# Performance work log

Measured on AMD Instinct MI355X. Metric: run time of the kernel, lower is better.

Reference implementation:

```python
import jax, jax.numpy as jnp
import numpy as np

HEAD, STACK = 8, 2
EPS = 1e-5


def _ln2d(x):
    # F.layer_norm(x, x.size()[1:]): normalize over (seq, feature) jointly, no affine
    m = jnp.mean(x, axis=(1, 2), keepdims=True)
    v = jnp.var(x, axis=(1, 2), keepdims=True)
    return (x - m) / jnp.sqrt(v + EPS)


def setup_inputs() -> dict:
    key = jax.random.key(0)
    ks = jax.random.split(key, 8)
    B, S, V, E, D, C = 64, 1024, 8000, 200, 200, 31
    g = lambda k, shape, sc: (jax.random.normal(k, shape, jnp.float32) * sc)
    return dict(
        x=jax.random.randint(ks[0], (B, S), 0, V),
        embed=g(ks[1], (V, E), 0.02),
        pos=g(ks[2], (S, E), 0.02),
        Wp=g(ks[3], (E, D), 0.05), bp=jnp.zeros((D,), jnp.float32),
        Wm=g(ks[4], (D * HEAD, D), 0.05), bm=jnp.zeros((D,), jnp.float32),
        W1=g(ks[5], (D, D), 0.05), b1=jnp.zeros((D,), jnp.float32),
        W2=g(ks[6], (D, D), 0.05), b2=jnp.zeros((D,), jnp.float32),
        Wd=g(ks[7], (D, C), 0.05), bd=jnp.zeros((C,), jnp.float32),
    )


def reference(x, embed, pos, Wp, bp, Wm, bm, W1, b1, W2, b2, Wd, bd):
    h = embed[x] + pos                       # [B,S,200]
    scale = jnp.sqrt(jnp.asarray(Wp.shape[1], jnp.float32))
    for _ in range(STACK):                   # weights shared across stacks (aliased in torch)
        r = h
        p = h @ Wp + bp                      # q = k = v (same aliased Linear in torch)
        a = jax.nn.softmax(jnp.einsum('bsd,btd->bst', p, p) / scale, axis=-1)
        c = jnp.einsum('bst,btd->bsd', a, p)  # [B,S,200]
        cat = jnp.tile(c, (1, 1, HEAD))       # all heads identical -> concat = tile
        h = _ln2d(cat @ Wm + bm + r)
        r = h
        ff = jax.nn.relu(h @ W1 + b1) @ W2 + b2
        h = _ln2d(ff + r)
    return h[:, -1, :] @ Wd + bd             # [B, class_num]; dropout = identity (eval)
```

## Files before the change

### kernel.cpp

```cpp
#include <hip/hip_runtime.h>
#include <cstddef>
#include <cstdint>
#include <cmath>

#define BDIM  64
#define SDIM  1024
#define DDIM  200
#define DPAD  224
#define PSTRIDE 232
#define CDIM  31
#define NSTACK 2
#define EPS   1e-5f
#define LN_N  204800.0f
#define PREP_BLOCKS 196

typedef __attribute__((ext_vector_type(8))) short short8;
typedef __attribute__((ext_vector_type(4))) short short4_t;
typedef __attribute__((ext_vector_type(4))) float f32x4;

__device__ __forceinline__ short f2bf(float f) {
    union { float f; unsigned u; } v; v.f = f;
    unsigned r = v.u + 0x7FFFu + ((v.u >> 16) & 1u);
    return (short)(r >> 16);
}
__device__ __forceinline__ float bf2f(short s) {
    union { unsigned u; float f; } v; v.u = ((unsigned)(unsigned short)s) << 16;
    return v.f;
}
__device__ __forceinline__ unsigned cvtpk_bf16(float a, float b) {
    unsigned r;
    asm volatile("v_cvt_pk_bf16_f32 %0, %1, %2" : "=v"(r) : "v"(a), "v"(b));
    return r;
}
__device__ __forceinline__ void gload_lds16(const short* g, short* l) {
    __builtin_amdgcn_global_load_lds(
        (const __attribute__((address_space(1))) void*)g,
        (__attribute__((address_space(3))) void*)l, 16, 0, 0);
}

__global__ void prep_embed_kernel(const int* __restrict__ x, const float* __restrict__ embed,
                                  const float* __restrict__ pos,
                                  const float* __restrict__ Wp, const float* __restrict__ bp,
                                  const float* __restrict__ Wm, const float* __restrict__ bm,
                                  const float* __restrict__ W1, const float* __restrict__ b1,
                                  const float* __restrict__ W2, const float* __restrict__ b2,
                                  short* __restrict__ WtP, short* __restrict__ WtM,
                                  short* __restrict__ Wt1, short* __restrict__ Wt2,
                                  float* __restrict__ bpP, float* __restrict__ bmP,
                                  float* __restrict__ b1P, float* __restrict__ b2P,
                                  float* __restrict__ csP, float* __restrict__ cs1,
                                  short* __restrict__ h, float* __restrict__ parts)
{
    if (blockIdx.x < PREP_BLOCKS) {
        int idx = blockIdx.x * 256 + threadIdx.x;
        if (idx >= DPAD * DPAD) return;
        int n = idx / DPAD, k = idx - n * DPAD;
        bool valid = (n < DDIM) && (k < DDIM);
        WtP[idx] = valid ? f2bf(Wp[(size_t)k * DDIM + n]) : 0;
        Wt1[idx] = valid ? f2bf(W1[(size_t)k * DDIM + n]) : 0;
        Wt2[idx] = valid ? f2bf(W2[(size_t)k * DDIM + n]) : 0;
        float s = 0.f;
        if (valid) {
            #pragma unroll
            for (int blk = 0; blk < 8; ++blk)
                s += Wm[(size_t)(blk * DDIM + k) * DDIM + n];
        }
        WtM[idx] = valid ? f2bf(s) : 0;
        if (idx < DPAD) {
            bpP[idx] = idx < DDIM ? bp[idx] : 0.f;
            bmP[idx] = idx < DDIM ? bm[idx] : 0.f;
            b1P[idx] = idx < DDIM ? b1[idx] : 0.f;
            b2P[idx] = idx < DDIM ? b2[idx] : 0.f;
            float sp = 0.f, s1 = 0.f;
            if (idx < DDIM) {
                for (int kk = 0; kk < DDIM; ++kk) {
                    sp += bf2f(f2bf(Wp[(size_t)kk * DDIM + idx]));
                    s1 += bf2f(f2bf(W1[(size_t)kk * DDIM + idx]));
                }
            }
            csP[idx] = sp;
            cs1[idx] = s1;
        }
        return;
    }

    const int eb = blockIdx.x - PREP_BLOCKS;
    if (eb == 0) {
        for (int i = threadIdx.x; i < 4 * BDIM * 2; i += 256) parts[i] = 0.f;
    }
    const int total = BDIM * SDIM * (DPAD / 4);
    for (int i = eb * 256 + threadIdx.x; i < total; i += 2048 * 256) {
        const int row = i / (DPAD / 4);
        const int n0  = (i - row * (DPAD / 4)) * 4;
        short4_t o;
        if (n0 >= DDIM) {
            o[0] = o[1] = o[2] = o[3] = 0;
        } else {
            const int s = row & (SDIM - 1);
            const int tok = x[row];
            const float4 e  = *(const float4*)(embed + (size_t)tok * DDIM + n0);
            const float4 p4 = *(const float4*)(pos + (size_t)s * DDIM + n0);
            o[0] = f2bf(e.x + p4.x); o[1] = f2bf(e.y + p4.y);
            o[2] = f2bf(e.z + p4.z); o[3] = f2bf(e.w + p4.w);
        }
        *(short4_t*)(h + (size_t)row * DPAD + n0) = o;
    }
}

#define WSLICE 7168
__global__ __launch_bounds__(256, 3)
void gemm_bf(const short* __restrict__ act, const float* __restrict__ actParts,
             const short* __restrict__ Wt, const float* __restrict__ bias,
             const float* __restrict__ csW,
             const short* __restrict__ res, const float* __restrict__ resParts,
             short* __restrict__ out, short* __restrict__ pt,
             float* __restrict__ parts, int doRelu, int outStride)
{
    __shared__ short WB[2][WSLICE];

    const int tid  = threadIdx.x;
    const int wave = tid >> 6, lane = tid & 63;
    const int lo   = lane & 15, hi = lane >> 4;
    const int mblk = blockIdx.x * 128;
    const int m0   = mblk + wave * 32;

    auto stage = [&](int ks, int buf) {
        for (int c = wave; c < 14; c += 4) {
            int row = c * 16 + (lane >> 2);
            int kc  = (lane & 3) ^ ((row >> 1) & 3);
            gload_lds16(Wt + (size_t)row * DPAD + ks * 32 + kc * 8,
                        &WB[buf][c * 512 + lane * 8]);
        }
    };

    f32x4 acc[2][14];
    #pragma unroll
    for (int mt = 0; mt < 2; ++mt)
        #pragma unroll
        for (int nt = 0; nt < 14; ++nt) acc[mt][nt] = (f32x4){0.f, 0.f, 0.f, 0.f};

    short8 af[2], afn[2];
    #pragma unroll
    for (int mt = 0; mt < 2; ++mt)
        af[mt] = *(const short8*)(act + (size_t)(m0 + mt * 16 + lo) * DPAD + hi * 8);
    stage(0, 0);
    __syncthreads();

    #pragma unroll
    for (int ks = 0; ks < 7; ++ks) {
        const int cur = ks & 1;
        if (ks < 6) {
            #pragma unroll
            for (int mt = 0; mt < 2; ++mt)
                afn[mt] = *(const short8*)(act + (size_t)(m0 + mt * 16 + lo) * DPAD
                                           + (ks + 1) * 32 + hi * 8);
            stage(ks + 1, cur ^ 1);
        }
        #pragma unroll
        for (int nt = 0; nt < 14; ++nt) {
            int brow = nt * 16 + lo;
            short8 bf_ = *(const short8*)&WB[cur][brow * 32
                                                  + ((hi * 8) ^ (((brow >> 1) & 3) << 3))];
            acc[0][nt] = __builtin_amdgcn_mfma_f32_16x16x32_bf16(af[0], bf_, acc[0][nt], 0, 0, 0);
            acc[1][nt] = __builtin_amdgcn_mfma_f32_16x16x32_bf16(af[1], bf_, acc[1][nt], 0, 0, 0);
        }
        __syncthreads();
        if (ks < 6) { af[0] = afn[0]; af[1] = afn[1]; }
    }

    const int bb = mblk >> 10;
    float inv_a = 1.f, corr = 0.f;
    if (actParts) {
        float mean = actParts[bb * 2] / LN_N;
        inv_a = rsqrtf(actParts[bb * 2 + 1] / LN_N - mean * mean + EPS);
        corr = mean * inv_a;
    }
    float mean_r = 0.f, inv_r = 1.f;
    if (resParts) {
        mean_r = resParts[bb * 2] / LN_N;
        inv_r = rsqrtf(resParts[bb * 2 + 1] / LN_N - mean_r * mean_r + EPS);
    }

    float s = 0.f, s2 = 0.f;
    #pragma unroll
    for (int mt = 0; mt < 2; ++mt) {
        #pragma unroll
        for (int nt = 0; nt < 14; ++nt) {
            const int n = nt * 16 + lo;
            const float bn = bias[n];
            const float cw = actParts ? csW[n] : 0.f;
            float v[4];
            #pragma unroll
            for (int r = 0; r < 4; ++r)
                v[r] = acc[mt][nt][r] * inv_a + bn - corr * cw;
            if (res) {
                #pragma unroll
                for (int r = 0; r < 4; ++r) {
                    int m = m0 + mt * 16 + hi * 4 + r;
                    v[r] += (bf2f(res[(size_t)m * DPAD + n]) - mean_r) * inv_r;
                }
            }
            if (doRelu)
                #pragma unroll
                for (int r = 0; r < 4; ++r) v[r] = fmaxf(v[r], 0.f);
            if (n >= DDIM)
                #pragma unroll
                for (int r = 0; r < 4; ++r) v[r] = 0.f;
            if (parts)
                #pragma unroll
                for (int r = 0; r < 4; ++r) { s += v[r]; s2 = fmaf(v[r], v[r], s2); }
            short4_t o4;
            #pragma unroll
            for (int r = 0; r < 4; ++r) o4[r] = f2bf(v[r]);
            #pragma unroll
            for (int r = 0; r < 4; ++r) {
                int m = m0 + mt * 16 + hi * 4 + r;
                out[(size_t)m * outStride + n] = o4[r];
            }
            if (pt && nt < 13) {
                const int sloc = (m0 + mt * 16 + hi * 4) & (SDIM - 1);
                *(short4_t*)(pt + ((size_t)bb * DPAD + n) * SDIM + sloc) = o4;
            }
        }
    }

    if (parts) {
        __shared__ float rs[4], rq[4];
        #pragma unroll
        for (int off = 32; off; off >>= 1) {
            s  += __shfl_down(s, off);
            s2 += __shfl_down(s2, off);
        }
        if (lane == 0) { rs[wave] = s; rq[wave] = s2; }
        __syncthreads();
        if (tid == 0) {
            atomicAdd(&parts[bb * 2],     rs[0] + rs[1] + rs[2] + rs[3]);
            atomicAdd(&parts[bb * 2 + 1], rq[0] + rq[1] + rq[2] + rq[3]);
        }
    }
}

#define Y1S 232
__global__ __launch_bounds__(256, 2)
void ffn_bf(const short* __restrict__ act, const float* __restrict__ actParts,
            const float* __restrict__ csW1,
            const short* __restrict__ Wt1, const float* __restrict__ b1,
            const short* __restrict__ Wt2, const float* __restrict__ b2,
            short* __restrict__ out, float* __restrict__ parts)
{
    __shared__ short WB[2][WSLICE];
    __shared__ short Y1[64 * Y1S];

    const int tid  = threadIdx.x;
    const int wave = tid >> 6, lane = tid & 63;
    const int lo   = lane & 15, hi = lane >> 4;
    const int mblk = blockIdx.x * 64;
    const int m0   = mblk + wave * 16;
    const int bb   = mblk >> 10;

    auto stageW = [&](const short* W, int ks, int buf) {
        for (int c = wave; c < 14; c += 4) {
            int row = c * 16 + (lane >> 2);
            int kc  = (lane & 3) ^ ((row >> 1) & 3);
            gload_lds16(W + (size_t)row * DPAD + ks * 32 + kc * 8,
                        &WB[buf][c * 512 + lane * 8]);
        }
    };

    const float mean_a = actParts[bb * 2] / LN_N;
    const float inv_a  = rsqrtf(actParts[bb * 2 + 1] / LN_N - mean_a * mean_a + EPS);
    const float corr   = mean_a * inv_a;

    f32x4 acc[14];
    #pragma unroll
    for (int nt = 0; nt < 14; ++nt) acc[nt] = (f32x4){0.f, 0.f, 0.f, 0.f};

    short8 af = *(const short8*)(act + (size_t)(m0 + lo) * DPAD + hi * 8);
    short8 afn;
    stageW(Wt1, 0, 0);
    __syncthreads();

    #pragma unroll
    for (int ks = 0; ks < 7; ++ks) {
        const int cur = ks & 1;
        if (ks < 6) {
            afn = *(const short8*)(act + (size_t)(m0 + lo) * DPAD + (ks + 1) * 32 + hi * 8);
            stageW(Wt1, ks + 1, cur ^ 1);
        } else {
            stageW(Wt2, 0, cur ^ 1);
        }
        #pragma unroll
        for (int nt = 0; nt < 14; ++nt) {
            int brow = nt * 16 + lo;
            short8 bf_ = *(const short8*)&WB[cur][brow * 32
                                                  + ((hi * 8) ^ (((brow >> 1) & 3) << 3))];
            acc[nt] = __builtin_amdgcn_mfma_f32_16x16x32_bf16(af, bf_, acc[nt], 0, 0, 0);
        }
        __syncthreads();
        if (ks < 6) af = afn;
    }

    #pragma unroll
    for (int nt = 0; nt < 14; ++nt) {
        const int n = nt * 16 + lo;
        const float bn = b1[n];
        const float cw = csW1[n];
        #pragma unroll
        for (int r = 0; r < 4; ++r) {
            float v = fmaxf(acc[nt][r] * inv_a + bn - corr * cw, 0.f);
            Y1[(wave * 16 + hi * 4 + r) * Y1S + n] = f2bf(v);
        }
    }
    __syncthreads();

    #pragma unroll
    for (int nt = 0; nt < 14; ++nt) acc[nt] = (f32x4){0.f, 0.f, 0.f, 0.f};

    #pragma unroll
    for (int ks = 0; ks < 7; ++ks) {
        const int cur = (ks + 1) & 1;
        if (ks < 6) stageW(Wt2, ks + 1, cur ^ 1);
        short8 a2 = *(const short8*)&Y1[(wave * 16 + lo) * Y1S + ks * 32 + hi * 8];
        #pragma unroll
        for (int nt = 0; nt < 14; ++nt) {
            int brow = nt * 16 + lo;
            short8 bf_ = *(const short8*)&WB[cur][brow * 32
                                                  + ((hi * 8) ^ (((brow >> 1) & 3) << 3))];
            acc[nt] = __builtin_amdgcn_mfma_f32_16x16x32_bf16(a2, bf_, acc[nt], 0, 0, 0);
        }
        __syncthreads();
    }

    float s = 0.f, s2 = 0.f;
    #pragma unroll
    for (int nt = 0; nt < 14; ++nt) {
        const int n = nt * 16 + lo;
        const float bn = b2[n];
        float v[4];
        #pragma unroll
        for (int r = 0; r < 4; ++r) {
            int m = m0 + hi * 4 + r;
            v[r] = acc[nt][r] + bn + (bf2f(act[(size_t)m * DPAD + n]) - mean_a) * inv_a;
        }
        if (n >= DDIM)
            #pragma unroll
            for (int r = 0; r < 4; ++r) v[r] = 0.f;
        #pragma unroll
        for (int r = 0; r < 4; ++r) { s += v[r]; s2 = fmaf(v[r], v[r], s2); }
        #pragma unroll
        for (int r = 0; r < 4; ++r) {
            int m = m0 + hi * 4 + r;
            out[(size_t)m * DPAD + n] = f2bf(v[r]);
        }
    }

    {
        __shared__ float rs[4], rq[4];
        #pragma unroll
        for (int off = 32; off; off >>= 1) {
            s  += __shfl_down(s, off);
            s2 += __shfl_down(s2, off);
        }
        if (lane == 0) { rs[wave] = s; rq[wave] = s2; }
        __syncthreads();
        if (tid == 0) {
            atomicAdd(&parts[bb * 2],     rs[0] + rs[1] + rs[2] + rs[3]);
            atomicAdd(&parts[bb * 2 + 1], rq[0] + rq[1] + rq[2] + rq[3]);
        }
    }
}

__global__ __launch_bounds__(256, 2)
void attn_kernel(const short* __restrict__ pbf, const short* __restrict__ pt,
                 short* __restrict__ c, float qscale)
{
    __shared__ short Kbuf[2][7680];
    __shared__ short Vbuf[2][6656];

    const int bid = blockIdx.x;
    const int wg  = (bid & 7) * 64 + (bid >> 3);
    const int b   = wg >> 3;
    const int q0  = (wg & 7) * 128;

    const int tid  = threadIdx.x;
    const int wave = tid >> 6;
    const int lane = tid & 63;
    const int lo   = lane & 15;
    const int hi   = lane >> 4;

    const short* pb  = pbf + (size_t)b * SDIM * PSTRIDE;
    const short* ptb = pt  + (size_t)b * DPAD * SDIM;

    auto stage = [&](int kt2, int bufIdx) {
        const short* ks = pb + (size_t)kt2 * 32 * PSTRIDE + lane * 8;
        #pragma unroll
        for (int i = 0; i < 15; ++i)
            gload_lds16(ks + i * 512, &Kbuf[bufIdx][i * 512]);
        #pragma unroll
        for (int i = 0; i < 13; ++i) {
            int e = i * 512 + lane * 8;
            int d = e >> 5;
            int cc = (e & 31) ^ (((d >> 1) & 3) << 3);
            gload_lds16(ptb + (size_t)d * SDIM + kt2 * 32 + cc, &Vbuf[bufIdx][i * 512]);
        }
    };

    short8 qf[2][7];
    #pragma unroll
    for (int qt = 0; qt < 2; ++qt)
        #pragma unroll
        for (int ks = 0; ks < 7; ++ks) {
            short8 q = *(const short8*)(pb + (size_t)(q0 + wave * 32 + qt * 16 + lo) * PSTRIDE
                                        + ks * 32 + hi * 8);
            short8 qs;
            #pragma unroll
            for (int j = 0; j < 8; ++j) qs[j] = f2bf(bf2f(q[j]) * qscale);
            qf[qt][ks] = qs;
        }

    f32x4 o[2][13];
    float m[2], ell[2];
    #pragma unroll
    for (int qt = 0; qt < 2; ++qt) {
        #pragma unroll
        for (int n = 0; n < 13; ++n) o[qt][n] = (f32x4){0.f, 0.f, 0.f, 0.f};
        m[qt] = -1e30f; ell[qt] = 0.f;
    }

    if (wave == 0) stage(0, 0);
    __syncthreads();

    for (int kt = 0; kt < 32; ++kt) {
        const int cur = kt & 1;
        if (kt < 31 && wave == ((kt + 1) & 3)) stage(kt + 1, cur ^ 1);

        f32x4 sacc[2][2];
        #pragma unroll
        for (int qt = 0; qt < 2; ++qt)
            #pragma unroll
            for (int t = 0; t < 2; ++t) sacc[qt][t] = (f32x4){0.f, 0.f, 0.f, 0.f};
        __builtin_amdgcn_s_setprio(1);
        #pragma unroll
        for (int t = 0; t < 2; ++t)
            #pragma unroll
            for (int ks = 0; ks < 7; ++ks) {
                short8 kf = *(const short8*)(&Kbuf[cur][(t * 16 + lo) * PSTRIDE + ks * 32 + hi * 8]);
                sacc[0][t] = __builtin_amdgcn_mfma_f32_16x16x32_bf16(kf, qf[0][ks], sacc[0][t], 0, 0, 0);
                sacc[1][t] = __builtin_amdgcn_mfma_f32_16x16x32_bf16(kf, qf[1][ks], sacc[1][t], 0, 0, 0);
            }
        __builtin_amdgcn_s_setprio(0);

        short8 pa[2];
        #pragma unroll
        for (int qt = 0; qt < 2; ++qt) {
            float mx = fmaxf(fmaxf(fmaxf(sacc[qt][0][0], sacc[qt][0][1]),
                                   fmaxf(sacc[qt][0][2], sacc[qt][0][3])),
                             fmaxf(fmaxf(sacc[qt][1][0], sacc[qt][1][1]),
                                   fmaxf(sacc[qt][1][2], sacc[qt][1][3])));
            mx = fmaxf(mx, __shfl_xor(mx, 16));
            mx = fmaxf(mx, __shfl_xor(mx, 32));
            if (__any(mx > m[qt] + 11.5f)) {
                float mn = fmaxf(m[qt], mx);
                float al = exp2f(m[qt] - mn);
                m[qt] = mn; ell[qt] *= al;
                float alr[4];
                #pragma unroll
                for (int r = 0; r < 4; ++r) alr[r] = __shfl(al, hi * 4 + r);
                #pragma unroll
                for (int n = 0; n < 13; ++n)
                    #pragma unroll
                    for (int r = 0; r < 4; ++r) o[qt][n][r] *= alr[r];
            }
            float p[2][4]; float rsum = 0.f;
            #pragma unroll
            for (int t = 0; t < 2; ++t)
                #pragma unroll
                for (int r = 0; r < 4; ++r) {
                    p[t][r] = exp2f(sacc[qt][t][r] - m[qt]);
                    rsum += p[t][r];
                }
            rsum += __shfl_xor(rsum, 16);
            rsum += __shfl_xor(rsum, 32);
            ell[qt] += rsum;
            unsigned pk01_0 = cvtpk_bf16(p[0][0], p[0][1]);
            unsigned pk23_0 = cvtpk_bf16(p[0][2], p[0][3]);
            unsigned pk01_1 = cvtpk_bf16(p[1][0], p[1][1]);
            unsigned pk23_1 = cvtpk_bf16(p[1][2], p[1][3]);
            const int srcA = lo + ((hi & 1) * 2) * 16;
            const int srcB = srcA + 16;
            int a0 = __shfl((int)pk01_0, srcA), a1 = __shfl((int)pk01_1, srcA);
            int b0 = __shfl((int)pk23_0, srcA), b1 = __shfl((int)pk23_1, srcA);
            int c0 = __shfl((int)pk01_0, srcB), c1 = __shfl((int)pk01_1, srcB);
            int d0 = __shfl((int)pk23_0, srcB), d1 = __shfl((int)pk23_1, srcB);
            const bool thi = (hi >> 1) != 0;
            union { short8 s; int u[4]; } pu;
            pu.u[0] = thi ? a1 : a0;
            pu.u[1] = thi ? b1 : b0;
            pu.u[2] = thi ? c1 : c0;
            pu.u[3] = thi ? d1 : d0;
            pa[qt] = pu.s;
        }

        __builtin_amdgcn_s_setprio(1);
        #pragma unroll
        for (int n = 0; n < 13; ++n) {
            int d = n * 16 + lo;
            int addr = d * 32 + ((hi * 8) ^ (((d >> 1) & 3) << 3));
            short8 vf = *(const short8*)(&Vbuf[cur][addr]);
            o[0][n] = __builtin_amdgcn_mfma_f32_16x16x32_bf16(pa[0], vf, o[0][n], 0, 0, 0);
            o[1][n] = __builtin_amdgcn_mfma_f32_16x16x32_bf16(pa[1], vf, o[1][n], 0, 0, 0);
        }
        __builtin_amdgcn_s_setprio(0);

        __syncthreads();
    }

    #pragma unroll
    for (int qt = 0; qt < 2; ++qt) {
        float inv_l = 1.f / ell[qt];
        float invr[4];
        #pragma unroll
        for (int r = 0; r < 4; ++r) invr[r] = __shfl(inv_l, hi * 4 + r);
        #pragma unroll
        for (int n = 0; n < 13; ++n) {
            int dcol = n * 16 + lo;
            #pragma unroll
            for (int r = 0; r < 4; ++r) {
                size_t row = (size_t)b * SDIM + q0 + wave * 32 + qt * 16 + hi * 4 + r;
                c[row * DPAD + dcol] = f2bf(o[qt][n][r] * invr[r]);
            }
        }
        #pragma unroll
        for (int r = 0; r < 4; ++r) {
            size_t row = (size_t)b * SDIM + q0 + wave * 32 + qt * 16 + hi * 4 + r;
            c[row * DPAD + 208 + lo] = 0;
        }
    }
}

__global__ void final_kernel(const short* __restrict__ y, const float* __restrict__ parts,
                             const float* __restrict__ Wd, const float* __restrict__ bd,
                             float* __restrict__ out)
{
    const int b = blockIdx.x;
    const float sum = parts[b * 2], sq = parts[b * 2 + 1];
    const float mean = sum / LN_N;
    const float inv  = rsqrtf(sq / LN_N - mean * mean + EPS);
    __shared__ float hrow[DDIM];
    const short* row = y + ((size_t)b * SDIM + SDIM - 1) * DPAD;
    for (int d = threadIdx.x; d < DDIM; d += blockDim.x)
        hrow[d] = (bf2f(row[d]) - mean) * inv;
    __syncthreads();
    if (threadIdx.x < CDIM) {
        float acc = bd[threadIdx.x];
        for (int d = 0; d < DDIM; ++d)
            acc = fmaf(hrow[d], Wd[(size_t)d * CDIM + threadIdx.x], acc);
        out[(size_t)b * CDIM + threadIdx.x] = acc;
    }
}

extern "C" void kernel_launch(void* const* d_in, const int* in_sizes, int n_in,
                              void* d_out, int out_size, void* d_ws, size_t ws_size,
                              hipStream_t stream)
{
    const int*   x     = (const int*)  d_in[0];
    const float* embed = (const float*)d_in[1];
    const float* pos   = (const float*)d_in[2];
    const float* Wp    = (const float*)d_in[3];
    const float* bp    = (const float*)d_in[4];
    const float* Wm    = (const float*)d_in[5];
    const float* bm    = (const float*)d_in[6];
    const float* W1    = (const float*)d_in[7];
    const float* b1    = (const float*)d_in[8];
    const float* W2    = (const float*)d_in[9];
    const float* b2    = (const float*)d_in[10];
    const float* Wd    = (const float*)d_in[11];
    const float* bd    = (const float*)d_in[12];
    float* out = (float*)d_out;

    const size_t HB = (size_t)BDIM * SDIM * DPAD;
    const size_t PB = (size_t)BDIM * SDIM * PSTRIDE;

    short* h_bf  = (short*)d_ws;
    short* p_bf  = h_bf  + HB;
    short* pt    = p_bf  + PB;
    short* cb_bf = pt    + HB;
    short* yA    = cb_bf + HB;
    short* yB    = yA    + HB;
    short* WtP   = yB + HB;
    short* WtM   = WtP + DPAD * DPAD;
    short* Wt1   = WtM + DPAD * DPAD;
    short* Wt2   = Wt1 + DPAD * DPAD;
    float* bpP   = (float*)(Wt2 + DPAD * DPAD);
    float* bmP   = bpP + DPAD;
    float* b1P   = bmP + DPAD;
    float* b2P   = b1P + DPAD;
    float* csP   = b2P + DPAD;
    float* cs1   = csP + DPAD;
    float* parts = cs1 + DPAD;
    const size_t need = (size_t)((char*)(parts + 4 * BDIM * 2) - (char*)d_ws);
    if (ws_size < need) return;

    float* pA1 = parts;
    float* pB1 = parts + BDIM * 2;
    float* pA2 = parts + 2 * BDIM * 2;
    float* pB2 = parts + 3 * BDIM * 2;

    prep_embed_kernel<<<dim3(PREP_BLOCKS + 2048), dim3(256), 0, stream>>>(
        x, embed, pos, Wp, bp, Wm, bm, W1, b1, W2, b2,
        WtP, WtM, Wt1, Wt2, bpP, bmP, b1P, b2P, csP, cs1, h_bf, parts);

    const float qscale = 1.44269504f / sqrtf((float)DDIM);

    gemm_bf<<<dim3(512), dim3(256), 0, stream>>>(h_bf, nullptr, WtP, bpP, nullptr,
                                                 nullptr, nullptr, p_bf, pt, nullptr, 0, PSTRIDE);
    attn_kernel<<<dim3(512), dim3(256), 0, stream>>>(p_bf, pt, cb_bf, qscale);
    gemm_bf<<<dim3(512), dim3(256), 0, stream>>>(cb_bf, nullptr, WtM, bmP, nullptr,
                                                 h_bf, nullptr, yA, nullptr, pA1, 0, DPAD);
    ffn_bf<<<dim3(1024), dim3(256), 0, stream>>>(yA, pA1, cs1, Wt1, b1P, Wt2, b2P, yB, pB1);
    gemm_bf<<<dim3(512), dim3(256), 0, stream>>>(yB, pB1, WtP, bpP, csP,
                                                 nullptr, nullptr, p_bf, pt, nullptr, 0, PSTRIDE);
    attn_kernel<<<dim3(512), dim3(256), 0, stream>>>(p_bf, pt, cb_bf, qscale);
    gemm_bf<<<dim3(512), dim3(256), 0, stream>>>(cb_bf, nullptr, WtM, bmP, nullptr,
                                                 yB, pB1, h_bf, nullptr, pA2, 0, DPAD);
    ffn_bf<<<dim3(1024), dim3(256), 0, stream>>>(h_bf, pA2, cs1, Wt1, b1P, Wt2, b2P, yA, pB2);
    final_kernel<<<dim3(BDIM), dim3(64), 0, stream>>>(yA, pB2, Wd, bd, out);
}
```

Before: 382.0 us.

## Triple-buffer weight slices with explicit vmcnt waits in GEMM and FFN kernels

Expands the LDS weight staging from double to triple buffering, so each K-slice is prefetched two iterations ahead. Full __syncthreads are replaced by manual s_waitcnt vmcnt counts plus s_barrier, letting some global-to-LDS loads stay in flight across barriers. The FFN kernel gets a unified stage index spanning both weight matrices so prefetch continues across the W1/W2 boundary. This uses more LDS per block, which may reduce occupancy, and the hand-counted vmcnt values could race if the compiler's load counts differ from what the code assumes.

```diff
diff --git a/kernel.cpp b/kernel.cpp
--- a/kernel.cpp
+++ b/kernel.cpp
@@ -116,7 +116,7 @@
              short* __restrict__ out, short* __restrict__ pt,
              float* __restrict__ parts, int doRelu, int outStride)
 {
-    __shared__ short WB[2][WSLICE];
+    __shared__ short WB[3][WSLICE];
 
     const int tid  = threadIdx.x;
     const int wave = tid >> 6, lane = tid & 63;
@@ -144,18 +144,21 @@
     for (int mt = 0; mt < 2; ++mt)
         af[mt] = *(const short8*)(act + (size_t)(m0 + mt * 16 + lo) * DPAD + hi * 8);
     stage(0, 0);
-    __syncthreads();
+    stage(1, 1);
+    asm volatile("s_waitcnt vmcnt(3)" ::: "memory");
+    __builtin_amdgcn_s_barrier();
 
     #pragma unroll
     for (int ks = 0; ks < 7; ++ks) {
-        const int cur = ks & 1;
+        const int cur = ks % 3;
         if (ks < 6) {
             #pragma unroll
             for (int mt = 0; mt < 2; ++mt)
                 afn[mt] = *(const short8*)(act + (size_t)(m0 + mt * 16 + lo) * DPAD
                                            + (ks + 1) * 32 + hi * 8);
-            stage(ks + 1, cur ^ 1);
-        }
+        }
+        if (ks < 5) stage(ks + 2, (ks + 2) % 3);
+
         #pragma unroll
         for (int nt = 0; nt < 14; ++nt) {
             int brow = nt * 16 + lo;
@@ -164,7 +167,9 @@
             acc[0][nt] = __builtin_amdgcn_mfma_f32_16x16x32_bf16(af[0], bf_, acc[0][nt], 0, 0, 0);
             acc[1][nt] = __builtin_amdgcn_mfma_f32_16x16x32_bf16(af[1], bf_, acc[1][nt], 0, 0, 0);
         }
-        __syncthreads();
+        if (ks < 5)       asm volatile("s_waitcnt vmcnt(5)" ::: "memory");
+        else if (ks == 5) asm volatile("s_waitcnt vmcnt(2)" ::: "memory");
+        if (ks < 6) __builtin_amdgcn_s_barrier();
         if (ks < 6) { af[0] = afn[0]; af[1] = afn[1]; }
     }
 
@@ -248,7 +253,7 @@
             const short* __restrict__ Wt2, const float* __restrict__ b2,
             short* __restrict__ out, float* __restrict__ parts)
 {
-    __shared__ short WB[2][WSLICE];
+    __shared__ short WB[3][WSLICE];
     __shared__ short Y1[64 * Y1S];
 
     const int tid  = threadIdx.x;
@@ -258,11 +263,14 @@
     const int m0   = mblk + wave * 16;
     const int bb   = mblk >> 10;
 
-    auto stageW = [&](const short* W, int ks, int buf) {
+    auto stageJ = [&](int j) {
+        const short* W = (j < 7) ? Wt1 : Wt2;
+        const int kk = (j < 7) ? j : j - 7;
+        const int buf = j % 3;
         for (int c = wave; c < 14; c += 4) {
             int row = c * 16 + (lane >> 2);
             int kc  = (lane & 3) ^ ((row >> 1) & 3);
-            gload_lds16(W + (size_t)row * DPAD + ks * 32 + kc * 8,
+            gload_lds16(W + (size_t)row * DPAD + kk * 32 + kc * 8,
                         &WB[buf][c * 512 + lane * 8]);
         }
     };
@@ -277,18 +285,17 @@
 
     short8 af = *(const short8*)(act + (size_t)(m0 + lo) * DPAD + hi * 8);
     short8 afn;
-    stageW(Wt1, 0, 0);
-    __syncthreads();
+    stageJ(0);
+    stageJ(1);
+    asm volatile("s_waitcnt vmcnt(3)" ::: "memory");
+    __builtin_amdgcn_s_barrier();
 
     #pragma unroll
     for (int ks = 0; ks < 7; ++ks) {
-        const int cur = ks & 1;
-        if (ks < 6) {
+        const int cur = ks % 3;
+        if (ks < 6)
             afn = *(const short8*)(act + (size_t)(m0 + lo) * DPAD + (ks + 1) * 32 + hi * 8);
-            stageW(Wt1, ks + 1, cur ^ 1);
-        } else {
-            stageW(Wt2, 0, cur ^ 1);
-        }
+        stageJ(ks + 2);
         #pragma unroll
         for (int nt = 0; nt < 14; ++nt) {
             int brow = nt * 16 + lo;
@@ -296,8 +303,11 @@
                                                   + ((hi * 8) ^ (((brow >> 1) & 3) << 3))];
             acc[nt] = __builtin_amdgcn_mfma_f32_16x16x32_bf16(af, bf_, acc[nt], 0, 0, 0);
         }
-        __syncthreads();
-        if (ks < 6) af = afn;
+        if (ks < 6) {
+            asm volatile("s_waitcnt vmcnt(5)" ::: "memory");
+            __builtin_amdgcn_s_barrier();
+            af = afn;
+        }
     }
 
     #pragma unroll
@@ -317,10 +327,10 @@
     for (int nt = 0; nt < 14; ++nt) acc[nt] = (f32x4){0.f, 0.f, 0.f, 0.f};
 
     #pragma unroll
-    for (int ks = 0; ks < 7; ++ks) {
-        const int cur = (ks + 1) & 1;
-        if (ks < 6) stageW(Wt2, ks + 1, cur ^ 1);
-        short8 a2 = *(const short8*)&Y1[(wave * 16 + lo) * Y1S + ks * 32 + hi * 8];
+    for (int j = 7; j < 14; ++j) {
+        const int cur = j % 3;
+        if (j < 12) stageJ(j + 2);
+        short8 a2 = *(const short8*)&Y1[(wave * 16 + lo) * Y1S + (j - 7) * 32 + hi * 8];
         #pragma unroll
         for (int nt = 0; nt < 14; ++nt) {
             int brow = nt * 16 + lo;
@@ -328,7 +338,9 @@
                                                   + ((hi * 8) ^ (((brow >> 1) & 3) << 3))];
             acc[nt] = __builtin_amdgcn_mfma_f32_16x16x32_bf16(a2, bf_, acc[nt], 0, 0, 0);
         }
-        __syncthreads();
+        if (j < 12)       asm volatile("s_waitcnt vmcnt(3)" ::: "memory");
+        else if (j == 12) asm volatile("s_waitcnt vmcnt(0)" ::: "memory");
+        if (j < 13) __builtin_amdgcn_s_barrier();
     }
 
     float s = 0.f, s2 = 0.f;
```

New measurement: 399.1 us. 1.04x slower.
